# Kernel tuning notes

Measured on AMD Instinct MI355X. Metric: run time of the kernel, lower is better.

Reference implementation:

```python
import jax, jax.numpy as jnp
import numpy as np

HEAD_SIZE = 128
N_Q_HEADS = 32
N_KV_HEADS = 8
ROPE_THETA = 1000000.0
RMS_EPS = 1e-6


def rms_norm(x, w, eps=RMS_EPS):
    # normalize over last dim in fp32, like Qwen3RMSNorm
    xf = x.astype(jnp.float32)
    var = jnp.mean(xf * xf, axis=-1, keepdims=True)
    return w * (xf * jax.lax.rsqrt(var + eps)).astype(x.dtype)


def rope_cache(T, dim, theta=ROPE_THETA):
    half = dim // 2
    inv_freq = 1.0 / theta ** (jnp.arange(half, dtype=jnp.float32) / half)
    freqs = jnp.arange(T, dtype=jnp.float32)[:, None] * inv_freq[None, :]  # [T, half]
    emb = jnp.concatenate([freqs, freqs], axis=-1)  # [T, dim]
    return jnp.cos(emb), jnp.sin(emb)


def rotate_half(x):
    x1, x2 = jnp.split(x, 2, axis=-1)
    return jnp.concatenate([-x2, x1], axis=-1)


def setup_inputs() -> dict:
    key = jax.random.key(0)
    ks = jax.random.split(key, 5)
    B, T, C = 2, 2048, 4096
    s = 0.02
    return {
        "hidden_states": jax.random.normal(ks[0], (B, T, C), jnp.float32),
        "wq": jax.random.normal(ks[1], (N_Q_HEADS * HEAD_SIZE, C), jnp.float32) * s,
        "wk": jax.random.normal(ks[2], (N_KV_HEADS * HEAD_SIZE, C), jnp.float32) * s,
        "wv": jax.random.normal(ks[3], (N_KV_HEADS * HEAD_SIZE, C), jnp.float32) * s,
        "wo": jax.random.normal(ks[4], (C, N_Q_HEADS * HEAD_SIZE), jnp.float32) * s,
        "q_norm_w": jnp.ones((HEAD_SIZE,), jnp.float32),
        "k_norm_w": jnp.ones((HEAD_SIZE,), jnp.float32),
    }


def reference(hidden_states, wq, wk, wv, wo, q_norm_w, k_norm_w):
    B, T, C = hidden_states.shape
    D = HEAD_SIZE
    groups = N_Q_HEADS // N_KV_HEADS
    scale = D ** -0.5

    # projections -> [B, H, T, D]
    q = (hidden_states @ wq.T).reshape(B, T, N_Q_HEADS, D)
    k = (hidden_states @ wk.T).reshape(B, T, N_KV_HEADS, D)
    v = (hidden_states @ wv.T).reshape(B, T, N_KV_HEADS, D)

    q = rms_norm(q, q_norm_w).transpose(0, 2, 1, 3)
    k = rms_norm(k, k_norm_w).transpose(0, 2, 1, 3)
    v = v.transpose(0, 2, 1, 3)

    cos, sin = rope_cache(T, D)  # [T, D]
    cos = cos[None, None]  # broadcast over batch, heads
    sin = sin[None, None]
    q = q * cos + rotate_half(q) * sin
    k = k * cos + rotate_half(k) * sin

    # GQA repeat_kv: [B, Hkv, T, D] -> [B, Hq, T, D]
    k = jnp.repeat(k, groups, axis=1)
    v = jnp.repeat(v, groups, axis=1)

    # causal SDPA
    scores = jnp.einsum("bhqd,bhkd->bhqk", q, k) * scale
    causal = jnp.tril(jnp.ones((T, T), bool))
    scores = jnp.where(causal[None, None], scores, -jnp.inf)
    probs = jax.nn.softmax(scores, axis=-1)
    attn = jnp.einsum("bhqk,bhkd->bhqd", probs, v)

    attn = attn.transpose(0, 2, 1, 3).reshape(B, T, N_Q_HEADS * D)
    return attn @ wo.T
```

## Files before the change

kernel.cpp:

```cpp
#include <hip/hip_runtime.h>
#include <math.h>

typedef unsigned short u16;
typedef __attribute__((ext_vector_type(8))) short short8;
typedef __attribute__((ext_vector_type(4))) float f32x4;
typedef __attribute__((ext_vector_type(16))) float f32x16;

#define AS1 __attribute__((address_space(1)))
#define AS3 __attribute__((address_space(3)))

__device__ __forceinline__ void gload_lds16(const u16* g, u16* l) {
  __builtin_amdgcn_global_load_lds((AS1 void*)g, (AS3 void*)l, 16, 0, 0);
}

__device__ __forceinline__ float bf2f(u16 u) {
  union { unsigned i; float f; } c; c.i = ((unsigned)u) << 16; return c.f;
}
__device__ __forceinline__ u16 f2bf(float f) {
  union { float f; unsigned i; } c; c.f = f;
  unsigned r = c.i + 0x7fffu + ((c.i >> 16) & 1u);
  return (u16)(r >> 16);
}

__global__ __launch_bounds__(256)
void cvt_f32_bf16_k(const float* __restrict__ src, u16* __restrict__ dst, int n8)
{
  int i = blockIdx.x * blockDim.x + threadIdx.x;
  const int stride = gridDim.x * blockDim.x;
  for (; i < n8; i += stride) {
    float4 a = ((const float4*)src)[2 * i];
    float4 b = ((const float4*)src)[2 * i + 1];
    short8 o;
    o[0] = (short)f2bf(a.x); o[1] = (short)f2bf(a.y);
    o[2] = (short)f2bf(a.z); o[3] = (short)f2bf(a.w);
    o[4] = (short)f2bf(b.x); o[5] = (short)f2bf(b.y);
    o[6] = (short)f2bf(b.z); o[7] = (short)f2bf(b.w);
    ((short8*)dst)[i] = o;
  }
}

template<int MODE, typename OutT>
__global__ __launch_bounds__(256, 2)
void gemm_bt(const u16* __restrict__ A, const u16* __restrict__ W0,
             const u16* __restrict__ W1, const u16* __restrict__ W2,
             OutT* __restrict__ C)
{
  constexpr int K = 4096;
  constexpr int LDC = (MODE == 0) ? 6144 : 4096;

  __shared__ __align__(16) u16 sA[128 * 32];
  __shared__ __align__(16) u16 sB[128 * 32];

  const int tid = threadIdx.x;
  const int wid = tid >> 6, lane = tid & 63;
  const int g = lane >> 4, li = lane & 15;
  const int bn = blockIdx.x, bm = blockIdx.y;
  const int wr = wid >> 1, wc = wid & 1;
  const int n0 = bn * 128;

  const u16* Wp; int nrow0;
  if (MODE == 0) {
    if (n0 < 4096)      { Wp = W0; nrow0 = n0; }
    else if (n0 < 5120) { Wp = W1; nrow0 = n0 - 4096; }
    else                { Wp = W2; nrow0 = n0 - 5120; }
  } else { Wp = W0; nrow0 = n0; }

  const u16* aptr = A  + (size_t)(bm * 128 + (tid >> 2)) * K + (tid & 3) * 8;
  const u16* bptr = Wp + (size_t)(nrow0   + (tid >> 2)) * K + (tid & 3) * 8;
  u16* sAw = sA + wid * 512;
  u16* sBw = sB + wid * 512;

  f32x4 acc[4][4] = {};

  for (int k0 = 0; k0 < K; k0 += 32) {
    gload_lds16(aptr + k0,           sAw);
    gload_lds16(aptr + k0 + 64 * K,  sAw + 2048);
    gload_lds16(bptr + k0,           sBw);
    gload_lds16(bptr + k0 + 64 * K,  sBw + 2048);
    __syncthreads();

    short8 af[4], bfv[4];
#pragma unroll
    for (int m = 0; m < 4; ++m)
      af[m]  = *(const short8*)(sA + (wr * 64 + m * 16 + li) * 32 + g * 8);
#pragma unroll
    for (int n = 0; n < 4; ++n)
      bfv[n] = *(const short8*)(sB + (wc * 64 + n * 16 + li) * 32 + g * 8);
#pragma unroll
    for (int m = 0; m < 4; ++m)
#pragma unroll
      for (int n = 0; n < 4; ++n)
        acc[m][n] = __builtin_amdgcn_mfma_f32_16x16x32_bf16(af[m], bfv[n], acc[m][n], 0, 0, 0);
    __syncthreads();
  }

#pragma unroll
  for (int m = 0; m < 4; ++m)
#pragma unroll
    for (int n = 0; n < 4; ++n)
#pragma unroll
      for (int j = 0; j < 4; ++j) {
        int row = bm * 128 + wr * 64 + m * 16 + g * 4 + j;
        int col = n0 + wc * 64 + n * 16 + li;
        float v = acc[m][n][j];
        if constexpr (sizeof(OutT) == 2) C[(size_t)row * LDC + col] = (OutT)f2bf(v);
        else                             C[(size_t)row * LDC + col] = (OutT)v;
      }
}

__global__ __launch_bounds__(256)
void norm_rope(const u16* __restrict__ qkv, const float* __restrict__ qw,
               const float* __restrict__ kw, u16* __restrict__ Qo,
               u16* __restrict__ Ko)
{
  const int tid = threadIdx.x;
  const int wid = tid >> 6, l = tid & 63;
  const int idx = blockIdx.x * 4 + wid;

  const u16* src; const float* w; u16* dst; int t;
  if (idx < 131072) {
    int row = idx >> 5, h = idx & 31;
    int b = row >> 11; t = row & 2047;
    src = qkv + (size_t)row * 6144 + h * 128;
    w = qw;
    dst = Qo + (((size_t)(b * 32 + h)) * 2048 + t) * 128;
  } else {
    int j = idx - 131072;
    int row = j >> 3, hk = j & 7;
    int b = row >> 11; t = row & 2047;
    src = qkv + (size_t)row * 6144 + 4096 + hk * 128;
    w = kw;
    dst = Ko + (((size_t)(b * 8 + hk)) * 2048 + t) * 128;
  }

  float x1 = bf2f(src[l]), x2 = bf2f(src[l + 64]);
  float ss = x1 * x1 + x2 * x2;
#pragma unroll
  for (int off = 32; off; off >>= 1) ss += __shfl_xor(ss, off);
  float rn = rsqrtf(ss * (1.0f / 128.0f) + 1e-6f);
  float y1 = x1 * rn * w[l];
  float y2 = x2 * rn * w[l + 64];

  float ang = (float)t * expf((float)l * -0.21586735246819178f);
  float c = cosf(ang), s = sinf(ang);
  dst[l]      = f2bf(y1 * c - y2 * s);
  dst[l + 64] = f2bf(y2 * c + y1 * s);
}

__global__ __launch_bounds__(256)
void transpose_v(const u16* __restrict__ qkv, u16* __restrict__ Vt)
{
  const int tblk = blockIdx.x, bh = blockIdx.y;
  const int b = bh >> 3, hk = bh & 7;
  const int tid = threadIdx.x;
  __shared__ __align__(16) u16 tile[64][136];

#pragma unroll
  for (int r = 0; r < 4; ++r) {
    int u = tid + r * 256;
    int row = u >> 4, cu = u & 15;
    short8 v = *(const short8*)(qkv + (size_t)(b * 2048 + tblk * 64 + row) * 6144
                                + 5120 + hk * 128 + cu * 8);
    *(short8*)(&tile[row][cu * 8]) = v;
  }
  __syncthreads();
#pragma unroll
  for (int it = 0; it < 4; ++it) {
    int u = tid + it * 256;
    int d = u & 127, tg = u >> 7;
    short8 wv8;
#pragma unroll
    for (int j = 0; j < 8; ++j) wv8[j] = (short)tile[tg * 8 + j][d];
    *(short8*)(Vt + ((size_t)(b * 8 + hk) * 128 + d) * 2048 + tblk * 64 + tg * 8) = wv8;
  }
}

__global__ __launch_bounds__(256, 2)
void attn_fwd(const u16* __restrict__ Q, const u16* __restrict__ Kc,
              const u16* __restrict__ Vt, u16* __restrict__ O)
{
  const int qt = 15 - (int)blockIdx.x;
  const int bh = blockIdx.y;
  const int b = bh >> 5, h = bh & 31, hkv = h >> 2;
  const int tid = threadIdx.x, wid = tid >> 6;
  const int lane = tid & 63, ql = lane & 31, hi = lane >> 5;

  __shared__ __align__(16) u16 sK[2][64 * 128];
  __shared__ __align__(16) u16 sV[2][128 * 64];

  const u16* Kb = Kc + ((size_t)(b * 8 + hkv)) * 2048 * 128;
  const u16* Vb = Vt + ((size_t)(b * 8 + hkv)) * 128 * 2048;

  const int kr0 = tid >> 4;
  const u16* kSrc = Kb + (size_t)kr0 * 128 + (((tid & 15) ^ (kr0 & 7)) * 8);
  const int vr0 = tid >> 3;
  const u16* vSrc = Vb + (size_t)vr0 * 2048 + (((tid & 7) ^ (vr0 & 7)) * 8);
  u16* const kDst = (u16*)sK[0] + wid * 512;
  u16* const vDst = (u16*)sV[0] + wid * 512;

  const int qg = qt * 128 + wid * 32 + ql;
  const u16* qrow = Q + ((size_t)(b * 32 + h) * 2048 + qg) * 128;
  short8 qf[8];
#pragma unroll
  for (int m = 0; m < 8; ++m) qf[m] = *(const short8*)(qrow + m * 16 + hi * 8);

  f32x16 oacc[4] = {};
  float mrun = -INFINITY, lrun = 0.f;
  const float scale = 0.08838834764831845f;
  const int nt = 2 * qt + 2;

#pragma unroll
  for (int p = 0; p < 4; ++p) {
    gload_lds16(kSrc + p * 2048,  kDst + p * 2048);
    gload_lds16(vSrc + p * 65536, vDst + p * 2048);
  }
  asm volatile("s_waitcnt vmcnt(0)" ::: "memory");
  __builtin_amdgcn_s_barrier();

  int cur = 0;
  for (int kt = 0; kt < nt; ++kt) {
    const int kv0 = kt * 64;
    if (kt + 1 < nt) {
      const u16* ks = kSrc + (size_t)(kv0 + 64) * 128;
      const u16* vs = vSrc + (kv0 + 64);
      u16* kd = kDst + (cur ^ 1) * 8192;
      u16* vd = vDst + (cur ^ 1) * 8192;
#pragma unroll
      for (int p = 0; p < 4; ++p) {
        gload_lds16(ks + p * 2048,  kd + p * 2048);
        gload_lds16(vs + p * 65536, vd + p * 2048);
      }
    }
    const u16* sKc = sK[cur];
    const u16* sVc = sV[cur];

    f32x16 P0 = {}, P1 = {};
    __builtin_amdgcn_s_setprio(1);
#pragma unroll
    for (int m = 0; m < 8; ++m) {
      const int c0 = ((m * 2 + hi) ^ (ql & 7)) * 8;
      short8 k0 = *(const short8*)(sKc + ql * 128 + c0);
      short8 k1 = *(const short8*)(sKc + (32 + ql) * 128 + c0);
      P0 = __builtin_amdgcn_mfma_f32_32x32x16_bf16(k0, qf[m], P0, 0, 0, 0);
      P1 = __builtin_amdgcn_mfma_f32_32x32x16_bf16(k1, qf[m], P1, 0, 0, 0);
    }
    __builtin_amdgcn_s_setprio(0);

#pragma unroll
    for (int r = 0; r < 16; ++r) {
      const int kvl = (r & 3) + 8 * (r >> 2) + 4 * hi;
      float v0 = P0[r] * scale; if (kv0 + kvl > qg)      v0 = -INFINITY; P0[r] = v0;
      float v1 = P1[r] * scale; if (kv0 + 32 + kvl > qg) v1 = -INFINITY; P1[r] = v1;
    }

    float pmax = -INFINITY;
#pragma unroll
    for (int r = 0; r < 16; ++r) pmax = fmaxf(pmax, fmaxf(P0[r], P1[r]));
    pmax = fmaxf(pmax, __shfl_xor(pmax, 32));

    if (!__all(pmax - mrun <= 8.f)) {
      float mnew = fmaxf(mrun, pmax);
      float corr = __expf(mrun - mnew);
      lrun *= corr;
      mrun = mnew;
#pragma unroll
      for (int r = 0; r < 16; ++r) {
        int qidx = (r & 3) + 8 * (r >> 2) + 4 * hi;
        float cr = __shfl(corr, qidx);
#pragma unroll
        for (int dt = 0; dt < 4; ++dt) oacc[dt][r] *= cr;
      }
    }

    float psum = 0.f;
#pragma unroll
    for (int r = 0; r < 16; ++r) {
      float e0 = __expf(P0[r] - mrun); P0[r] = e0; psum += e0;
      float e1 = __expf(P1[r] - mrun); P1[r] = e1; psum += e1;
    }
    psum += __shfl_xor(psum, 32);
    lrun += psum;

    __builtin_amdgcn_s_setprio(1);
#pragma unroll
    for (int s = 0; s < 4; ++s) {
      const int R0 = 8 * (s & 1), R1 = R0 + 4;
      float a0 = (s < 2) ? P0[R0 + 0] : P1[R0 + 0];
      float a1 = (s < 2) ? P0[R0 + 1] : P1[R0 + 1];
      float a2 = (s < 2) ? P0[R0 + 2] : P1[R0 + 2];
      float a3 = (s < 2) ? P0[R0 + 3] : P1[R0 + 3];
      float b0 = (s < 2) ? P0[R1 + 0] : P1[R1 + 0];
      float b1 = (s < 2) ? P0[R1 + 1] : P1[R1 + 1];
      float b2 = (s < 2) ? P0[R1 + 2] : P1[R1 + 2];
      float b3 = (s < 2) ? P0[R1 + 3] : P1[R1 + 3];
      unsigned y0, y1, z0, z1;
      asm("v_cvt_pk_bf16_f32 %0, %1, %2" : "=v"(y0) : "v"(a0), "v"(a1));
      asm("v_cvt_pk_bf16_f32 %0, %1, %2" : "=v"(z0) : "v"(b0), "v"(b1));
      asm("v_cvt_pk_bf16_f32 %0, %1, %2" : "=v"(y1) : "v"(a2), "v"(a3));
      asm("v_cvt_pk_bf16_f32 %0, %1, %2" : "=v"(z1) : "v"(b2), "v"(b3));
      asm("v_permlane32_swap_b32 %0, %1" : "+v"(y0), "+v"(z0));
      asm("v_permlane32_swap_b32 %0, %1" : "+v"(y1), "+v"(z1));
      union { unsigned u[4]; short8 v; } pa;
      pa.u[0] = y0; pa.u[1] = y1; pa.u[2] = z0; pa.u[3] = z1;
#pragma unroll
      for (int dt = 0; dt < 4; ++dt) {
        const int c = ((s * 2 + hi) ^ (ql & 7)) * 8;
        short8 vf = *(const short8*)(sVc + (dt * 32 + ql) * 64 + c);
        oacc[dt] = __builtin_amdgcn_mfma_f32_32x32x16_bf16(pa.v, vf, oacc[dt], 0, 0, 0);
      }
    }
    __builtin_amdgcn_s_setprio(0);

    asm volatile("s_waitcnt lgkmcnt(0)" ::: "memory");
    asm volatile("s_waitcnt vmcnt(0)" ::: "memory");
    __builtin_amdgcn_s_barrier();
    cur ^= 1;
  }

  float inv = 1.f / lrun;
  const int qbase = b * 2048 + qt * 128 + wid * 32;
#pragma unroll
  for (int r = 0; r < 16; ++r) {
    const int qidx = (r & 3) + 8 * (r >> 2) + 4 * hi;
    float ir = __shfl(inv, qidx);
    size_t base = (size_t)(qbase + qidx) * 4096 + h * 128 + ql;
#pragma unroll
    for (int dt = 0; dt < 4; ++dt)
      O[base + dt * 32] = f2bf(oacc[dt][r] * ir);
  }
}

extern "C" void kernel_launch(void* const* d_in, const int* in_sizes, int n_in,
                              void* d_out, int out_size, void* d_ws, size_t ws_size,
                              hipStream_t stream) {
  const float* hs  = (const float*)d_in[0];
  const float* wq  = (const float*)d_in[1];
  const float* wk  = (const float*)d_in[2];
  const float* wv  = (const float*)d_in[3];
  const float* wo  = (const float*)d_in[4];
  const float* qnw = (const float*)d_in[5];
  const float* knw = (const float*)d_in[6];
  float* out = (float*)d_out;

  char* ws = (char*)d_ws;
  u16* qkv = (u16*)(ws);
  u16* qr  = (u16*)(ws + 50331648);
  u16* kr  = (u16*)(ws + 83886080);
  u16* vt  = (u16*)(ws + 92274688);
  u16* hsb = (u16*)(ws + 100663296);
  u16* wqb = (u16*)(ws + 134217728);
  u16* wkb = (u16*)(ws + 167772160);
  u16* wvb = (u16*)(ws + 176160768);
  u16* ao  = (u16*)(ws);
  u16* wob = qr;

  cvt_f32_bf16_k<<<dim3(2048), dim3(256), 0, stream>>>(hs, hsb, 16777216 / 8);
  cvt_f32_bf16_k<<<dim3(2048), dim3(256), 0, stream>>>(wq, wqb, 16777216 / 8);
  cvt_f32_bf16_k<<<dim3(1024), dim3(256), 0, stream>>>(wk, wkb, 4194304 / 8);
  cvt_f32_bf16_k<<<dim3(1024), dim3(256), 0, stream>>>(wv, wvb, 4194304 / 8);

  gemm_bt<0, u16><<<dim3(48, 32), dim3(256), 0, stream>>>(hsb, wqb, wkb, wvb, qkv);
  norm_rope<<<dim3(40960), dim3(256), 0, stream>>>(qkv, qnw, knw, qr, kr);
  transpose_v<<<dim3(32, 16), dim3(256), 0, stream>>>(qkv, vt);
  attn_fwd<<<dim3(16, 64), dim3(256), 0, stream>>>(qr, kr, vt, ao);

  cvt_f32_bf16_k<<<dim3(2048), dim3(256), 0, stream>>>(wo, wob, 16777216 / 8);
  gemm_bt<1, float><<<dim3(32, 32), dim3(256), 0, stream>>>(ao, wob, nullptr, nullptr, out);
}
```

Baseline: 641.5 us.

## Replace GEMM with 256x256 tiled, double-buffered, swizzled LDS pipeline

Replaces the 128x128 single-buffered GEMM with a 512-thread 256x256 tile kernel. It uses double-buffered LDS with XOR-swizzled layout, a K-step of 64, and staggered async global-to-LDS prefetch interleaved with MFMA phases. It also remaps block IDs for L2 locality and raises wave priority around MFMA bursts. The goals are to cut global traffic per FLOP, hide load latency and avoid LDS bank conflicts. The cost is much more LDS (128KB per block) and register pressure, with fewer blocks in flight.

```diff
diff --git a/kernel.cpp b/kernel.cpp
--- a/kernel.cpp
+++ b/kernel.cpp
@@ -39,24 +39,61 @@
   }
 }
 
+#define MFMA16(a, b, c) __builtin_amdgcn_mfma_f32_16x16x32_bf16((a), (b), (c), 0, 0, 0)
+
+#define STAGE_H(panel, h, t, ldsb)                                          \
+  { const u16* s_ = (panel) + (size_t)((h) * 128) * 4096 + (t) * 64;        \
+    gload_lds16(s_,                   (ldsb) + ldst0);                      \
+    gload_lds16(s_ + (size_t)64*4096, (ldsb) + 4096 + ldst0); }
+
+#define PHASE(MB, STAGE_STMT, TAIL)                                         \
+  {                                                                         \
+    short8 a0k0 = *(const short8*)(aB + (MB)*1024 + aoff0);                 \
+    short8 a0k1 = *(const short8*)(aB + (MB)*1024 + (aoff0 ^ 32));          \
+    short8 a1k0 = *(const short8*)(aB + ((MB)+1)*1024 + aoff0);             \
+    short8 a1k1 = *(const short8*)(aB + ((MB)+1)*1024 + (aoff0 ^ 32));      \
+    STAGE_STMT                                                              \
+    __builtin_amdgcn_s_barrier();                                           \
+    asm volatile("s_waitcnt lgkmcnt(0)" ::: "memory");                      \
+    __builtin_amdgcn_sched_barrier(0);                                      \
+    __builtin_amdgcn_s_setprio(1);                                          \
+    _Pragma("unroll")                                                       \
+    for (int n = 0; n < 4; ++n) {                                           \
+      acc[(MB)][n]   = MFMA16(a0k0, br[n][0], acc[(MB)][n]);                \
+      acc[(MB)][n]   = MFMA16(a0k1, br[n][1], acc[(MB)][n]);                \
+      acc[(MB)+1][n] = MFMA16(a1k0, br[n][0], acc[(MB)+1][n]);              \
+      acc[(MB)+1][n] = MFMA16(a1k1, br[n][1], acc[(MB)+1][n]);              \
+    }                                                                       \
+    __builtin_amdgcn_s_setprio(0);                                          \
+    TAIL                                                                    \
+    __builtin_amdgcn_s_barrier();                                           \
+  }
+
 template<int MODE, typename OutT>
-__global__ __launch_bounds__(256, 2)
-void gemm_bt(const u16* __restrict__ A, const u16* __restrict__ W0,
+__global__ __launch_bounds__(512, 2)
+void gemm256(const u16* __restrict__ A, const u16* __restrict__ W0,
              const u16* __restrict__ W1, const u16* __restrict__ W2,
              OutT* __restrict__ C)
 {
   constexpr int K = 4096;
+  constexpr int NT = K / 64;
   constexpr int LDC = (MODE == 0) ? 6144 : 4096;
-
-  __shared__ __align__(16) u16 sA[128 * 32];
-  __shared__ __align__(16) u16 sB[128 * 32];
+  constexpr int NBM = 16;
+  constexpr int NBN = (MODE == 0) ? 24 : 16;
+  constexpr int NWG = NBM * NBN;
+
+  __shared__ __align__(16) u16 sA[2 * 16384];
+  __shared__ __align__(16) u16 sB[2 * 16384];
 
   const int tid = threadIdx.x;
   const int wid = tid >> 6, lane = tid & 63;
   const int g = lane >> 4, li = lane & 15;
-  const int bn = blockIdx.x, bm = blockIdx.y;
-  const int wr = wid >> 1, wc = wid & 1;
-  const int n0 = bn * 128;
+  const int wr = wid >> 2, wc = wid & 3;
+
+  const int bid = blockIdx.x;
+  const int wg = (bid & 7) * (NWG / 8) + (bid >> 3);
+  const int bm = wg % NBM, bn = wg / NBM;
+  const int n0 = bn * 256;
 
   const u16* Wp; int nrow0;
   if (MODE == 0) {
@@ -65,42 +102,55 @@
     else                { Wp = W2; nrow0 = n0 - 5120; }
   } else { Wp = W0; nrow0 = n0; }
 
-  const u16* aptr = A  + (size_t)(bm * 128 + (tid >> 2)) * K + (tid & 3) * 8;
-  const u16* bptr = Wp + (size_t)(nrow0   + (tid >> 2)) * K + (tid & 3) * 8;
-  u16* sAw = sA + wid * 512;
-  u16* sBw = sB + wid * 512;
-
-  f32x4 acc[4][4] = {};
-
-  for (int k0 = 0; k0 < K; k0 += 32) {
-    gload_lds16(aptr + k0,           sAw);
-    gload_lds16(aptr + k0 + 64 * K,  sAw + 2048);
-    gload_lds16(bptr + k0,           sBw);
-    gload_lds16(bptr + k0 + 64 * K,  sBw + 2048);
-    __syncthreads();
-
-    short8 af[4], bfv[4];
-#pragma unroll
-    for (int m = 0; m < 4; ++m)
-      af[m]  = *(const short8*)(sA + (wr * 64 + m * 16 + li) * 32 + g * 8);
+  const int r0 = tid >> 3;
+  const int sc0 = (tid & 7) ^ (r0 & 7);
+  const u16* aS = A  + (size_t)(bm * 256 + r0) * K + sc0 * 8;
+  const u16* bS = Wp + (size_t)(nrow0   + r0) * K + sc0 * 8;
+  const int ldst0 = wid * 512;
+
+  const int aoff0 = li * 64 + ((g ^ (li & 7)) * 8);
+  const int boff0 = (wc & 1) * 4096 + aoff0;
+
+  f32x4 acc[8][4] = {};
+
+  STAGE_H(bS, 0, 0, sB);
+  STAGE_H(bS, 1, 0, sB + 8192);
+  STAGE_H(aS, 0, 0, sA);
+  STAGE_H(aS, 1, 0, sA + 8192);
+  STAGE_H(bS, 0, 1, sB + 16384);
+  STAGE_H(bS, 1, 1, sB + 24576);
+  asm volatile("s_waitcnt vmcnt(4)" ::: "memory");
+  __builtin_amdgcn_s_barrier();
+
+  for (int t = 0; t < NT; ++t) {
+    const int buf = t & 1;
+    const u16* aB = sA + buf * 16384 + wr * 8192;
+    const u16* bB = sB + buf * 16384 + (wc >> 1) * 8192;
+    u16* aO = sA + (buf ^ 1) * 16384;
+    u16* bO = sB + buf * 16384;
+    const bool st1 = (t + 1 < NT), st2 = (t + 2 < NT);
+
+    short8 br[4][2];
+#pragma unroll
+    for (int n = 0; n < 4; ++n) {
+      br[n][0] = *(const short8*)(bB + n * 1024 + boff0);
+      br[n][1] = *(const short8*)(bB + n * 1024 + (boff0 ^ 32));
+    }
+    PHASE(0, if (st1) STAGE_H(aS, 0, t + 1, aO);, ;)
+    PHASE(2, if (st1) STAGE_H(aS, 1, t + 1, aO + 8192);, ;)
+    PHASE(4, if (st2) STAGE_H(bS, 0, t + 2, bO);, ;)
+    PHASE(6, if (st2) STAGE_H(bS, 1, t + 2, bO + 8192);,
+          if (t < NT - 2) { asm volatile("s_waitcnt vmcnt(4)" ::: "memory"); }
+          else            { asm volatile("s_waitcnt vmcnt(0)" ::: "memory"); })
+  }
+
+#pragma unroll
+  for (int m = 0; m < 8; ++m)
 #pragma unroll
     for (int n = 0; n < 4; ++n)
-      bfv[n] = *(const short8*)(sB + (wc * 64 + n * 16 + li) * 32 + g * 8);
-#pragma unroll
-    for (int m = 0; m < 4; ++m)
-#pragma unroll
-      for (int n = 0; n < 4; ++n)
-        acc[m][n] = __builtin_amdgcn_mfma_f32_16x16x32_bf16(af[m], bfv[n], acc[m][n], 0, 0, 0);
-    __syncthreads();
-  }
-
-#pragma unroll
-  for (int m = 0; m < 4; ++m)
-#pragma unroll
-    for (int n = 0; n < 4; ++n)
 #pragma unroll
       for (int j = 0; j < 4; ++j) {
-        int row = bm * 128 + wr * 64 + m * 16 + g * 4 + j;
+        int row = bm * 256 + wr * 128 + m * 16 + g * 4 + j;
         int col = n0 + wc * 64 + n * 16 + li;
         float v = acc[m][n][j];
         if constexpr (sizeof(OutT) == 2) C[(size_t)row * LDC + col] = (OutT)f2bf(v);
@@ -359,11 +409,11 @@
   cvt_f32_bf16_k<<<dim3(1024), dim3(256), 0, stream>>>(wk, wkb, 4194304 / 8);
   cvt_f32_bf16_k<<<dim3(1024), dim3(256), 0, stream>>>(wv, wvb, 4194304 / 8);
 
-  gemm_bt<0, u16><<<dim3(48, 32), dim3(256), 0, stream>>>(hsb, wqb, wkb, wvb, qkv);
+  gemm256<0, u16><<<dim3(384), dim3(512), 0, stream>>>(hsb, wqb, wkb, wvb, qkv);
   norm_rope<<<dim3(40960), dim3(256), 0, stream>>>(qkv, qnw, knw, qr, kr);
   transpose_v<<<dim3(32, 16), dim3(256), 0, stream>>>(qkv, vt);
   attn_fwd<<<dim3(16, 64), dim3(256), 0, stream>>>(qr, kr, vt, ao);
 
   cvt_f32_bf16_k<<<dim3(2048), dim3(256), 0, stream>>>(wo, wob, 16777216 / 8);
-  gemm_bt<1, float><<<dim3(32, 32), dim3(256), 0, stream>>>(ao, wob, nullptr, nullptr, out);
-}
+  gemm256<1, float><<<dim3(256), dim3(512), 0, stream>>>(ao, wob, nullptr, nullptr, out);
+}
```

After: 655.0 us. +2.1%, slower.
